# Kernel optimization log

Hardware: AMD Instinct MI355X
Metric: run time of the kernel (lower is better)

Reference implementation:

```python
import jax, jax.numpy as jnp
import numpy as np

B, A, L, D, H = 8, 16, 80, 128, 6  # scenes, agents/scene, lanes/scene, feat dim, heads
LN_EPS = 1e-5


def _build_edges():
    hi_l, wi_l = [], []
    n_agt = B * A
    for b in range(B):
        ids = np.concatenate([np.arange(b * A, (b + 1) * A),
                              n_agt + np.arange(b * L, (b + 1) * L)])
        n = len(ids)
        hi_l.append(np.repeat(ids, n))  # 'd -> (d n)'
        wi_l.append(np.tile(ids, n))    # 'd -> (n d)'
    return (jnp.asarray(np.concatenate(hi_l), dtype=jnp.int32),
            jnp.asarray(np.concatenate(wi_l), dtype=jnp.int32))


def setup_inputs() -> dict:
    key = jax.random.key(0)
    ks = jax.random.split(key, 10)
    w = 0.05  # small init so exp(att) is well-behaved
    hi, wi = _build_edges()
    return {
        "agents": jax.random.normal(ks[0], (B * A, D), jnp.float32),
        "lanes": jax.random.normal(ks[1], (B * L, D), jnp.float32),
        "Wq": w * jax.random.normal(ks[2], (D, H * D), jnp.float32),
        "Wk": w * jax.random.normal(ks[3], (D, H * D), jnp.float32),
        "Wv": w * jax.random.normal(ks[4], (D, H * D), jnp.float32),
        "Wout1": w * jax.random.normal(ks[5], (H * D, D), jnp.float32),
        "Wout2": w * jax.random.normal(ks[6], (D, D), jnp.float32),
        "W1": w * jax.random.normal(ks[7], (D, D), jnp.float32),
        "ln_g": jnp.ones((D,), jnp.float32),
        "ln_b": jnp.zeros((D,), jnp.float32),
        "W2": w * jax.random.normal(ks[8], (D, D), jnp.float32),
        "hi": hi,
        "wi": wi,
    }


def _layernorm(x, g, b):
    mu = x.mean(-1, keepdims=True)
    var = ((x - mu) ** 2).mean(-1, keepdims=True)
    return (x - mu) * jax.lax.rsqrt(var + LN_EPS) * g + b


def reference(agents, lanes, Wq, Wk, Wv, Wout1, Wout2, W1, ln_g, ln_b, W2, hi, wi):
    nodes = jnp.concatenate([agents, lanes], axis=0)  # [N, D]
    N = nodes.shape[0]
    n_agt = agents.shape[0]
    scale = D ** -0.5

    src = nodes[hi]  # [E, D] (query side)
    dst = nodes[wi]  # [E, D] (key/value side)
    q = (src @ Wq).reshape(-1, H, D)
    k = (dst @ Wk).reshape(-1, H, D)
    v = jax.nn.relu(dst @ Wv).reshape(-1, H, D)

    att = jnp.einsum('ehd,ehd->eh', q, k) * scale          # [E, H]
    att = jnp.exp(att - att.max())                          # global-max-shifted exp (as in source)
    denom = jax.ops.segment_sum(att, hi, num_segments=N)    # [N, H]
    att = att / denom[hi]
    out = jax.ops.segment_sum(att[..., None] * v, hi, num_segments=N)  # [N, H, D]
    out = out.reshape(N, H * D)

    out = jax.nn.relu(out @ Wout1) @ Wout2                  # to_out
    h = _layernorm(nodes @ W1 + out, ln_g, ln_b)
    h = jax.nn.relu(h)
    h = h @ W2
    h = jax.nn.relu(h + nodes)                              # residual to pre-attention nodes
    return h[:n_agt]
```

## Files before the change

kernel.cpp:

```cpp
#include <hip/hip_runtime.h>
#include <math.h>

#define LN_EPS 1e-5f


__global__ __launch_bounds__(256) void k_qv(
    const float* __restrict__ agents, const float* __restrict__ lanes,
    const float* __restrict__ Wv, const float* __restrict__ Wq,
    float* __restrict__ V, float* __restrict__ Qb)
{
    __shared__ float As[128][68];
    __shared__ float Bs[128][68];

    const int tid = threadIdx.x;
    const int bid = blockIdx.x;

    const float* W;
    float* Out;
    int r0, wc0;
    bool dorelu = false;
    if (bid < 144) {
        const int br = bid % 12, bc = bid / 12;
        r0 = br * 64; W = Wv; wc0 = bc * 64;
        Out = V; dorelu = true;
    } else {
        const int idx = bid - 144;
        r0 = (idx & 1) * 64; W = Wq; wc0 = (idx >> 1) * 64;
        Out = Qb;
    }

    {
        const int row = tid >> 2, kv = tid & 3;
        const int gr = r0 + row;
        const float* src = (gr < 128) ? (agents + (size_t)gr * 128)
                                      : (lanes + (size_t)(gr - 128) * 128);
        #pragma unroll
        for (int j = 0; j < 8; ++j) {
            const int k0 = kv * 4 + j * 16;
            const float4 a = *(const float4*)(src + k0);
            As[k0 + 0][row] = a.x; As[k0 + 1][row] = a.y;
            As[k0 + 2][row] = a.z; As[k0 + 3][row] = a.w;
        }
    }
    {
        const int kr = tid >> 4, c4 = tid & 15;
        #pragma unroll
        for (int i = 0; i < 8; ++i) {
            const int k = kr + 16 * i;
            *(float4*)&Bs[k][c4 * 4] =
                *(const float4*)(W + (size_t)k * 768 + wc0 + c4 * 4);
        }
    }
    __syncthreads();

    const int tx = tid & 15, ty = tid >> 4;
    float acc[4][4] = {};
    #pragma unroll 8
    for (int k = 0; k < 128; ++k) {
        const float4 a = *(const float4*)&As[k][ty * 4];
        const float4 b = *(const float4*)&Bs[k][tx * 4];
        const float av[4] = {a.x, a.y, a.z, a.w};
        #pragma unroll
        for (int i = 0; i < 4; ++i) {
            acc[i][0] += av[i] * b.x; acc[i][1] += av[i] * b.y;
            acc[i][2] += av[i] * b.z; acc[i][3] += av[i] * b.w;
        }
    }
    #pragma unroll
    for (int i = 0; i < 4; ++i) {
        float4 v = make_float4(acc[i][0], acc[i][1], acc[i][2], acc[i][3]);
        if (dorelu) {
            v.x = fmaxf(v.x, 0.f); v.y = fmaxf(v.y, 0.f);
            v.z = fmaxf(v.z, 0.f); v.w = fmaxf(v.w, 0.f);
        }
        *(float4*)(Out + (size_t)(r0 + ty * 4 + i) * 768 + wc0 + tx * 4) = v;
    }
}

__global__ __launch_bounds__(512) void k_attn(
    const float* __restrict__ agents, const float* __restrict__ lanes,
    const float* __restrict__ Wk, const float* __restrict__ V,
    const float* __restrict__ Qb, float* __restrict__ AO)
{
    __shared__ float Ns[96][132];
    __shared__ float Vh[96][64];
    __shared__ float Qs[16][132];
    __shared__ float Tt[16][132];
    __shared__ float Wks[128][132];
    float (*Sm)[100] = (float (*)[100])&Wks[0][0];

    const int tid = threadIdx.x;
    const int b = blockIdx.x;
    const int s = b / 12, r12 = b % 12;
    const int h = r12 >> 1, half = r12 & 1;

    #pragma unroll
    for (int ii = 0; ii < 6; ++ii) {
        const int idx = tid + ii * 512;
        const int n = idx >> 5, c4 = idx & 31;
        const float* src = (n < 16) ? (agents + (size_t)(s * 16 + n) * 128)
                                    : (lanes + (size_t)(s * 80 + n - 16) * 128);
        *(float4*)&Ns[n][c4 * 4] = *(const float4*)(src + c4 * 4);
    }
    #pragma unroll
    for (int ii = 0; ii < 8; ++ii) {
        const int idx = tid + ii * 512;
        const int row = idx >> 5, c4 = idx & 31;
        *(float4*)&Wks[row][c4 * 4] =
            *(const float4*)(Wk + (size_t)row * 768 + h * 128 + c4 * 4);
    }
    #pragma unroll
    for (int ii = 0; ii < 3; ++ii) {
        const int idx = tid + ii * 512;
        const int n = idx >> 4, c4 = idx & 15;
        const int g = (n < 16) ? (s * 16 + n) : (128 + s * 80 + (n - 16));
        *(float4*)&Vh[n][c4 * 4] =
            *(const float4*)(V + (size_t)g * 768 + h * 128 + half * 64 + c4 * 4);
    }
    {
        const int r = tid >> 5, c4 = tid & 31;
        *(float4*)&Qs[r][c4 * 4] =
            *(const float4*)(Qb + (size_t)(s * 16 + r) * 768 + h * 128 + c4 * 4);
    }
    __syncthreads();

    if (tid < 128) {
        const int kc = tid & 31, rq = tid >> 5;
        float acc[4][4] = {};
        #pragma unroll 4
        for (int c4 = 0; c4 < 32; ++c4) {
            float4 q[4], w[4];
            #pragma unroll
            for (int u = 0; u < 4; ++u)
                q[u] = *(const float4*)&Qs[rq + 4 * u][c4 * 4];
            #pragma unroll
            for (int u = 0; u < 4; ++u)
                w[u] = *(const float4*)&Wks[kc + 32 * u][c4 * 4];
            #pragma unroll
            for (int ur = 0; ur < 4; ++ur)
                #pragma unroll
                for (int uk = 0; uk < 4; ++uk)
                    acc[ur][uk] += q[ur].x * w[uk].x + q[ur].y * w[uk].y
                                 + q[ur].z * w[uk].z + q[ur].w * w[uk].w;
        }
        #pragma unroll
        for (int ur = 0; ur < 4; ++ur)
            #pragma unroll
            for (int uk = 0; uk < 4; ++uk)
                Tt[rq + 4 * ur][kc + 32 * uk] = acc[ur][uk];
    }
    __syncthreads();

    if (tid < 128) {
        const int jc = tid & 31, iq = tid >> 5;
        float s0[4] = {}, s1[4] = {}, s2[4] = {};
        #pragma unroll 4
        for (int kk = 0; kk < 32; ++kk) {
            float4 t[4];
            #pragma unroll
            for (int u = 0; u < 4; ++u)
                t[u] = *(const float4*)&Tt[iq + 4 * u][kk * 4];
            const float4 n0 = *(const float4*)&Ns[jc][kk * 4];
            const float4 n1 = *(const float4*)&Ns[jc + 32][kk * 4];
            const float4 n2 = *(const float4*)&Ns[jc + 64][kk * 4];
            #pragma unroll
            for (int u = 0; u < 4; ++u) {
                s0[u] += t[u].x*n0.x + t[u].y*n0.y + t[u].z*n0.z + t[u].w*n0.w;
                s1[u] += t[u].x*n1.x + t[u].y*n1.y + t[u].z*n1.z + t[u].w*n1.w;
                s2[u] += t[u].x*n2.x + t[u].y*n2.y + t[u].z*n2.z + t[u].w*n2.w;
            }
        }
        const float scale = 0.088388347648318447f;
        #pragma unroll
        for (int u = 0; u < 4; ++u) {
            const float a0 = s0[u] * scale, a1 = s1[u] * scale, a2 = s2[u] * scale;
            float m = fmaxf(fmaxf(a0, a1), a2);
            #pragma unroll
            for (int o = 16; o >= 1; o >>= 1) m = fmaxf(m, __shfl_xor(m, o, 32));
            const float e0 = __expf(a0 - m), e1 = __expf(a1 - m), e2 = __expf(a2 - m);
            float sum = e0 + e1 + e2;
            #pragma unroll
            for (int o = 16; o >= 1; o >>= 1) sum += __shfl_xor(sum, o, 32);
            const float inv = 1.0f / sum;
            Sm[iq + 4 * u][jc]      = e0 * inv;
            Sm[iq + 4 * u][jc + 32] = e1 * inv;
            Sm[iq + 4 * u][jc + 64] = e2 * inv;
        }
    }
    __syncthreads();

    if (tid < 64) {
        const int d4 = tid & 15, iq = tid >> 4;
        float4 acc[4] = {};
        #pragma unroll 2
        for (int j = 0; j < 96; ++j) {
            const float4 v = *(const float4*)&Vh[j][d4 * 4];
            #pragma unroll
            for (int u = 0; u < 4; ++u) {
                const float p = Sm[iq + 4 * u][j];
                acc[u].x += p * v.x; acc[u].y += p * v.y;
                acc[u].z += p * v.z; acc[u].w += p * v.w;
            }
        }
        #pragma unroll
        for (int u = 0; u < 4; ++u)
            *(float4*)(AO + (size_t)(s * 16 + iq + 4 * u) * 768 +
                       h * 128 + half * 64 + d4 * 4) = acc[u];
    }
}

__global__ __launch_bounds__(512) void k_tail(
    const float* __restrict__ AO, const float* __restrict__ agents,
    const float* __restrict__ Wout1, const float* __restrict__ Wout2,
    const float* __restrict__ W1, const float* __restrict__ ln_g,
    const float* __restrict__ ln_b, const float* __restrict__ W2,
    float* __restrict__ out)
{
    __shared__ float ao[768];
    __shared__ float nrs[128];
    __shared__ float ps[2048];
    __shared__ float y1s[128];
    __shared__ float hb[128];
    __shared__ float red[4];

    const int a = blockIdx.x, tid = threadIdx.x;
    if (tid < 192) {
        *(float4*)&ao[tid * 4] = *(const float4*)(AO + (size_t)a * 768 + tid * 4);
    } else if (tid < 224) {
        const int t = tid - 192;
        *(float4*)&nrs[t * 4] = *(const float4*)(agents + (size_t)a * 128 + t * 4);
    }
    __syncthreads();

    const int d4 = tid & 31, g = tid >> 5;
    {
        float4 acc = make_float4(0, 0, 0, 0);
        const int k0 = g * 48;
        #pragma unroll 8
        for (int k = 0; k < 48; ++k) {
            const float av = ao[k0 + k];
            const float4 w = *(const float4*)(Wout1 + (size_t)(k0 + k) * 128 + d4 * 4);
            acc.x += av * w.x; acc.y += av * w.y;
            acc.z += av * w.z; acc.w += av * w.w;
        }
        *(float4*)&ps[g * 128 + d4 * 4] = acc;
    }
    __syncthreads();
    if (tid < 128) {
        float ssum = 0.f;
        #pragma unroll
        for (int gg = 0; gg < 16; ++gg) ssum += ps[gg * 128 + tid];
        y1s[tid] = fmaxf(ssum, 0.f);
    }
    __syncthreads();
    {
        float4 acc = make_float4(0, 0, 0, 0);
        const int k0 = g * 8;
        #pragma unroll
        for (int k = 0; k < 8; ++k) {
            const float yv = y1s[k0 + k], nv = nrs[k0 + k];
            const float4 w2v = *(const float4*)(Wout2 + (size_t)(k0 + k) * 128 + d4 * 4);
            const float4 w1v = *(const float4*)(W1 + (size_t)(k0 + k) * 128 + d4 * 4);
            acc.x += yv * w2v.x + nv * w1v.x; acc.y += yv * w2v.y + nv * w1v.y;
            acc.z += yv * w2v.z + nv * w1v.z; acc.w += yv * w2v.w + nv * w1v.w;
        }
        *(float4*)&ps[g * 128 + d4 * 4] = acc;
    }
    __syncthreads();
    float tval = 0.f;
    if (tid < 128) {
        #pragma unroll
        for (int gg = 0; gg < 16; ++gg) tval += ps[gg * 128 + tid];
    }
    float s1 = tval, s2 = tval * tval;
    #pragma unroll
    for (int o = 32; o >= 1; o >>= 1) { s1 += __shfl_xor(s1, o); s2 += __shfl_xor(s2, o); }
    if (tid < 128 && (tid & 63) == 0) {
        red[(tid >> 6) * 2] = s1; red[(tid >> 6) * 2 + 1] = s2;
    }
    __syncthreads();
    if (tid < 128) {
        const float S1 = red[0] + red[2], S2 = red[1] + red[3];
        const float mu  = S1 * (1.0f / 128.0f);
        const float var = S2 * (1.0f / 128.0f) - mu * mu;
        hb[tid] = fmaxf((tval - mu) * rsqrtf(var + LN_EPS) * ln_g[tid] + ln_b[tid], 0.f);
    }
    __syncthreads();
    {
        float4 acc = make_float4(0, 0, 0, 0);
        const int k0 = g * 8;
        #pragma unroll
        for (int k = 0; k < 8; ++k) {
            const float hv = hb[k0 + k];
            const float4 w = *(const float4*)(W2 + (size_t)(k0 + k) * 128 + d4 * 4);
            acc.x += hv * w.x; acc.y += hv * w.y;
            acc.z += hv * w.z; acc.w += hv * w.w;
        }
        *(float4*)&ps[g * 128 + d4 * 4] = acc;
    }
    __syncthreads();
    if (tid < 128) {
        float o_ = nrs[tid];
        #pragma unroll
        for (int gg = 0; gg < 16; ++gg) o_ += ps[gg * 128 + tid];
        out[(size_t)a * 128 + tid] = fmaxf(o_, 0.f);
    }
}

extern "C" void kernel_launch(void* const* d_in, const int* in_sizes, int n_in,
                              void* d_out, int out_size, void* d_ws, size_t ws_size,
                              hipStream_t stream)
{
    const float* agents = (const float*)d_in[0];
    const float* lanes  = (const float*)d_in[1];
    const float* Wq     = (const float*)d_in[2];
    const float* Wk     = (const float*)d_in[3];
    const float* Wv     = (const float*)d_in[4];
    const float* Wout1  = (const float*)d_in[5];
    const float* Wout2  = (const float*)d_in[6];
    const float* W1     = (const float*)d_in[7];
    const float* ln_g   = (const float*)d_in[8];
    const float* ln_b   = (const float*)d_in[9];
    const float* W2     = (const float*)d_in[10];

    float* ws = (float*)d_ws;
    float* V    = ws;
    float* Qb   = V + 768 * 768;
    float* AO   = Qb + 128 * 768;
    float* outp = (float*)d_out;

    k_qv  <<<168, 256, 0, stream>>>(agents, lanes, Wv, Wq, V, Qb);
    k_attn<<<96, 512, 0, stream>>>(agents, lanes, Wk, V, Qb, AO);
    k_tail<<<128, 512, 0, stream>>>(AO, agents, Wout1, Wout2, W1, ln_g, ln_b, W2, outp);
}
```

Baseline: 112.4 us.

## Fuse three kernels into one persistent kernel with atomic-counter grid barriers

Merges the QV projection, attention and tail kernels into a single launch of 168 blocks. Stages are separated by global atomic counters and spin-waits, with a shared-memory union reused across stages. The Wk and node loads are issued before the wait so they overlap the projection stage. The tail now handles two agents per block, and the probability matrix is stored transposed so the PV loop can use vector reads. This removes two kernel-launch gaps, but adds a memset launch and relies on all 168 blocks being co-resident for the spin barrier to be safe.

```diff
diff --git a/kernel.cpp b/kernel.cpp
--- a/kernel.cpp
+++ b/kernel.cpp
@@ -4,94 +4,109 @@
 #define LN_EPS 1e-5f
 
 
-__global__ __launch_bounds__(256) void k_qv(
+union SmemU {
+    struct {
+        float As[128][68];
+        float Bs[128][68];
+    } a;
+    struct {
+        float Ns[96][132];
+        float Wks[128][132];
+        float Vh[96][64];
+        float Qs[16][132];
+        float Tt[16][132];
+    } b;
+    struct {
+        float ao0[768], ao1[768];
+        float nr0[128], nr1[128];
+        float ps0[2048], ps1[2048];
+        float y10[128], y11[128];
+        float hb0[128], hb1[128];
+        float red[8];
+    } c;
+};
+
+__global__ __launch_bounds__(512) void k_all(
     const float* __restrict__ agents, const float* __restrict__ lanes,
-    const float* __restrict__ Wv, const float* __restrict__ Wq,
-    float* __restrict__ V, float* __restrict__ Qb)
+    const float* __restrict__ Wq, const float* __restrict__ Wk,
+    const float* __restrict__ Wv, const float* __restrict__ Wout1,
+    const float* __restrict__ Wout2, const float* __restrict__ W1,
+    const float* __restrict__ ln_g, const float* __restrict__ ln_b,
+    const float* __restrict__ W2, float* __restrict__ V,
+    float* __restrict__ Qb, float* __restrict__ AO,
+    int* __restrict__ cnts, float* __restrict__ out)
 {
-    __shared__ float As[128][68];
-    __shared__ float Bs[128][68];
-
+    __shared__ SmemU sm;
     const int tid = threadIdx.x;
     const int bid = blockIdx.x;
 
-    const float* W;
-    float* Out;
-    int r0, wc0;
-    bool dorelu = false;
-    if (bid < 144) {
-        const int br = bid % 12, bc = bid / 12;
-        r0 = br * 64; W = Wv; wc0 = bc * 64;
-        Out = V; dorelu = true;
+    if (tid < 256) {
+        const float* W;
+        float* Out;
+        int r0, wc0;
+        bool dorelu = false;
+        if (bid < 144) {
+            const int br = bid % 12, bc = bid / 12;
+            r0 = br * 64; W = Wv; wc0 = bc * 64; Out = V; dorelu = true;
+        } else {
+            const int idx = bid - 144;
+            r0 = (idx & 1) * 64; W = Wq; wc0 = (idx >> 1) * 64; Out = Qb;
+        }
+        {
+            const int row = tid >> 2, kv = tid & 3;
+            const int gr = r0 + row;
+            const float* src = (gr < 128) ? (agents + (size_t)gr * 128)
+                                          : (lanes + (size_t)(gr - 128) * 128);
+            #pragma unroll
+            for (int j = 0; j < 8; ++j) {
+                const int k0 = kv * 4 + j * 16;
+                const float4 a = *(const float4*)(src + k0);
+                sm.a.As[k0 + 0][row] = a.x; sm.a.As[k0 + 1][row] = a.y;
+                sm.a.As[k0 + 2][row] = a.z; sm.a.As[k0 + 3][row] = a.w;
+            }
+        }
+        {
+            const int kr = tid >> 4, c4 = tid & 15;
+            #pragma unroll
+            for (int i = 0; i < 8; ++i) {
+                const int k = kr + 16 * i;
+                *(float4*)&sm.a.Bs[k][c4 * 4] =
+                    *(const float4*)(W + (size_t)k * 768 + wc0 + c4 * 4);
+            }
+        }
+        __syncthreads();
+        const int tx = tid & 15, ty = tid >> 4;
+        float acc[4][4] = {};
+        #pragma unroll 8
+        for (int k = 0; k < 128; ++k) {
+            const float4 a = *(const float4*)&sm.a.As[k][ty * 4];
+            const float4 b = *(const float4*)&sm.a.Bs[k][tx * 4];
+            const float av[4] = {a.x, a.y, a.z, a.w};
+            #pragma unroll
+            for (int i = 0; i < 4; ++i) {
+                acc[i][0] += av[i] * b.x; acc[i][1] += av[i] * b.y;
+                acc[i][2] += av[i] * b.z; acc[i][3] += av[i] * b.w;
+            }
+        }
+        #pragma unroll
+        for (int i = 0; i < 4; ++i) {
+            float4 v = make_float4(acc[i][0], acc[i][1], acc[i][2], acc[i][3]);
+            if (dorelu) {
+                v.x = fmaxf(v.x, 0.f); v.y = fmaxf(v.y, 0.f);
+                v.z = fmaxf(v.z, 0.f); v.w = fmaxf(v.w, 0.f);
+            }
+            *(float4*)(Out + (size_t)(r0 + ty * 4 + i) * 768 + wc0 + tx * 4) = v;
+        }
     } else {
-        const int idx = bid - 144;
-        r0 = (idx & 1) * 64; W = Wq; wc0 = (idx >> 1) * 64;
-        Out = Qb;
-    }
-
-    {
-        const int row = tid >> 2, kv = tid & 3;
-        const int gr = r0 + row;
-        const float* src = (gr < 128) ? (agents + (size_t)gr * 128)
-                                      : (lanes + (size_t)(gr - 128) * 128);
-        #pragma unroll
-        for (int j = 0; j < 8; ++j) {
-            const int k0 = kv * 4 + j * 16;
-            const float4 a = *(const float4*)(src + k0);
-            As[k0 + 0][row] = a.x; As[k0 + 1][row] = a.y;
-            As[k0 + 2][row] = a.z; As[k0 + 3][row] = a.w;
-        }
-    }
-    {
-        const int kr = tid >> 4, c4 = tid & 15;
-        #pragma unroll
-        for (int i = 0; i < 8; ++i) {
-            const int k = kr + 16 * i;
-            *(float4*)&Bs[k][c4 * 4] =
-                *(const float4*)(W + (size_t)k * 768 + wc0 + c4 * 4);
-        }
-    }
-    __syncthreads();
-
-    const int tx = tid & 15, ty = tid >> 4;
-    float acc[4][4] = {};
-    #pragma unroll 8
-    for (int k = 0; k < 128; ++k) {
-        const float4 a = *(const float4*)&As[k][ty * 4];
-        const float4 b = *(const float4*)&Bs[k][tx * 4];
-        const float av[4] = {a.x, a.y, a.z, a.w};
-        #pragma unroll
-        for (int i = 0; i < 4; ++i) {
-            acc[i][0] += av[i] * b.x; acc[i][1] += av[i] * b.y;
-            acc[i][2] += av[i] * b.z; acc[i][3] += av[i] * b.w;
-        }
-    }
-    #pragma unroll
-    for (int i = 0; i < 4; ++i) {
-        float4 v = make_float4(acc[i][0], acc[i][1], acc[i][2], acc[i][3]);
-        if (dorelu) {
-            v.x = fmaxf(v.x, 0.f); v.y = fmaxf(v.y, 0.f);
-            v.z = fmaxf(v.z, 0.f); v.w = fmaxf(v.w, 0.f);
-        }
-        *(float4*)(Out + (size_t)(r0 + ty * 4 + i) * 768 + wc0 + tx * 4) = v;
-    }
-}
-
-__global__ __launch_bounds__(512) void k_attn(
-    const float* __restrict__ agents, const float* __restrict__ lanes,
-    const float* __restrict__ Wk, const float* __restrict__ V,
-    const float* __restrict__ Qb, float* __restrict__ AO)
-{
-    __shared__ float Ns[96][132];
-    __shared__ float Vh[96][64];
-    __shared__ float Qs[16][132];
-    __shared__ float Tt[16][132];
-    __shared__ float Wks[128][132];
-    float (*Sm)[100] = (float (*)[100])&Wks[0][0];
-
-    const int tid = threadIdx.x;
-    const int b = blockIdx.x;
-    const int s = b / 12, r12 = b % 12;
+        __syncthreads();
+    }
+
+    __threadfence();
+    __syncthreads();
+    if (tid == 0) atomicAdd(&cnts[0], 1);
+    if (bid >= 96) return;
+
+    const int s = bid / 12, r12 = bid % 12;
     const int h = r12 >> 1, half = r12 & 1;
 
     #pragma unroll
@@ -100,26 +115,36 @@
         const int n = idx >> 5, c4 = idx & 31;
         const float* src = (n < 16) ? (agents + (size_t)(s * 16 + n) * 128)
                                     : (lanes + (size_t)(s * 80 + n - 16) * 128);
-        *(float4*)&Ns[n][c4 * 4] = *(const float4*)(src + c4 * 4);
+        *(float4*)&sm.b.Ns[n][c4 * 4] = *(const float4*)(src + c4 * 4);
     }
     #pragma unroll
     for (int ii = 0; ii < 8; ++ii) {
         const int idx = tid + ii * 512;
         const int row = idx >> 5, c4 = idx & 31;
-        *(float4*)&Wks[row][c4 * 4] =
+        *(float4*)&sm.b.Wks[row][c4 * 4] =
             *(const float4*)(Wk + (size_t)row * 768 + h * 128 + c4 * 4);
     }
+
+    if (tid == 0) {
+        int guard = 0;
+        while (atomicAdd(&cnts[0], 0) < 168 && guard < 10000000) {
+            __builtin_amdgcn_s_sleep(2); ++guard;
+        }
+    }
+    __syncthreads();
+    __threadfence();
+
     #pragma unroll
     for (int ii = 0; ii < 3; ++ii) {
         const int idx = tid + ii * 512;
         const int n = idx >> 4, c4 = idx & 15;
         const int g = (n < 16) ? (s * 16 + n) : (128 + s * 80 + (n - 16));
-        *(float4*)&Vh[n][c4 * 4] =
+        *(float4*)&sm.b.Vh[n][c4 * 4] =
             *(const float4*)(V + (size_t)g * 768 + h * 128 + half * 64 + c4 * 4);
     }
     {
         const int r = tid >> 5, c4 = tid & 31;
-        *(float4*)&Qs[r][c4 * 4] =
+        *(float4*)&sm.b.Qs[r][c4 * 4] =
             *(const float4*)(Qb + (size_t)(s * 16 + r) * 768 + h * 128 + c4 * 4);
     }
     __syncthreads();
@@ -132,10 +157,10 @@
             float4 q[4], w[4];
             #pragma unroll
             for (int u = 0; u < 4; ++u)
-                q[u] = *(const float4*)&Qs[rq + 4 * u][c4 * 4];
+                q[u] = *(const float4*)&sm.b.Qs[rq + 4 * u][c4 * 4];
             #pragma unroll
             for (int u = 0; u < 4; ++u)
-                w[u] = *(const float4*)&Wks[kc + 32 * u][c4 * 4];
+                w[u] = *(const float4*)&sm.b.Wks[kc + 32 * u][c4 * 4];
             #pragma unroll
             for (int ur = 0; ur < 4; ++ur)
                 #pragma unroll
@@ -147,10 +172,11 @@
         for (int ur = 0; ur < 4; ++ur)
             #pragma unroll
             for (int uk = 0; uk < 4; ++uk)
-                Tt[rq + 4 * ur][kc + 32 * uk] = acc[ur][uk];
-    }
-    __syncthreads();
-
+                sm.b.Tt[rq + 4 * ur][kc + 32 * uk] = acc[ur][uk];
+    }
+    __syncthreads();
+
+    float (*Sm)[20] = (float (*)[20])&sm.b.Wks[0][0];
     if (tid < 128) {
         const int jc = tid & 31, iq = tid >> 5;
         float s0[4] = {}, s1[4] = {}, s2[4] = {};
@@ -159,10 +185,10 @@
             float4 t[4];
             #pragma unroll
             for (int u = 0; u < 4; ++u)
-                t[u] = *(const float4*)&Tt[iq + 4 * u][kk * 4];
-            const float4 n0 = *(const float4*)&Ns[jc][kk * 4];
-            const float4 n1 = *(const float4*)&Ns[jc + 32][kk * 4];
-            const float4 n2 = *(const float4*)&Ns[jc + 64][kk * 4];
+                t[u] = *(const float4*)&sm.b.Tt[iq + 4 * u][kk * 4];
+            const float4 n0 = *(const float4*)&sm.b.Ns[jc][kk * 4];
+            const float4 n1 = *(const float4*)&sm.b.Ns[jc + 32][kk * 4];
+            const float4 n2 = *(const float4*)&sm.b.Ns[jc + 64][kk * 4];
             #pragma unroll
             for (int u = 0; u < 4; ++u) {
                 s0[u] += t[u].x*n0.x + t[u].y*n0.y + t[u].z*n0.z + t[u].w*n0.w;
@@ -182,9 +208,10 @@
             #pragma unroll
             for (int o = 16; o >= 1; o >>= 1) sum += __shfl_xor(sum, o, 32);
             const float inv = 1.0f / sum;
-            Sm[iq + 4 * u][jc]      = e0 * inv;
-            Sm[iq + 4 * u][jc + 32] = e1 * inv;
-            Sm[iq + 4 * u][jc + 64] = e2 * inv;
+            const int i = iq + 4 * u;
+            Sm[jc][i]      = e0 * inv;
+            Sm[jc + 32][i] = e1 * inv;
+            Sm[jc + 64][i] = e2 * inv;
         }
     }
     __syncthreads();
@@ -194,116 +221,145 @@
         float4 acc[4] = {};
         #pragma unroll 2
         for (int j = 0; j < 96; ++j) {
-            const float4 v = *(const float4*)&Vh[j][d4 * 4];
+            const float4 p = *(const float4*)&Sm[j][iq * 4];
+            const float4 v = *(const float4*)&sm.b.Vh[j][d4 * 4];
+            const float pv[4] = {p.x, p.y, p.z, p.w};
             #pragma unroll
             for (int u = 0; u < 4; ++u) {
-                const float p = Sm[iq + 4 * u][j];
-                acc[u].x += p * v.x; acc[u].y += p * v.y;
-                acc[u].z += p * v.z; acc[u].w += p * v.w;
+                acc[u].x += pv[u] * v.x; acc[u].y += pv[u] * v.y;
+                acc[u].z += pv[u] * v.z; acc[u].w += pv[u] * v.w;
             }
         }
         #pragma unroll
         for (int u = 0; u < 4; ++u)
-            *(float4*)(AO + (size_t)(s * 16 + iq + 4 * u) * 768 +
+            *(float4*)(AO + (size_t)(s * 16 + iq * 4 + u) * 768 +
                        h * 128 + half * 64 + d4 * 4) = acc[u];
     }
-}
-
-__global__ __launch_bounds__(512) void k_tail(
-    const float* __restrict__ AO, const float* __restrict__ agents,
-    const float* __restrict__ Wout1, const float* __restrict__ Wout2,
-    const float* __restrict__ W1, const float* __restrict__ ln_g,
-    const float* __restrict__ ln_b, const float* __restrict__ W2,
-    float* __restrict__ out)
-{
-    __shared__ float ao[768];
-    __shared__ float nrs[128];
-    __shared__ float ps[2048];
-    __shared__ float y1s[128];
-    __shared__ float hb[128];
-    __shared__ float red[4];
-
-    const int a = blockIdx.x, tid = threadIdx.x;
+
+    __threadfence();
+    __syncthreads();
+    if (tid == 0) atomicAdd(&cnts[1 + s], 1);
+    if (r12 >= 8) return;
+
+    if (tid == 0) {
+        int guard = 0;
+        while (atomicAdd(&cnts[1 + s], 0) < 12 && guard < 10000000) {
+            __builtin_amdgcn_s_sleep(2); ++guard;
+        }
+    }
+    __syncthreads();
+    __threadfence();
+
+    const int a0 = s * 16 + r12 * 2, a1 = a0 + 1;
     if (tid < 192) {
-        *(float4*)&ao[tid * 4] = *(const float4*)(AO + (size_t)a * 768 + tid * 4);
-    } else if (tid < 224) {
+        *(float4*)&sm.c.ao0[tid * 4] = *(const float4*)(AO + (size_t)a0 * 768 + tid * 4);
+    } else if (tid < 384) {
         const int t = tid - 192;
-        *(float4*)&nrs[t * 4] = *(const float4*)(agents + (size_t)a * 128 + t * 4);
+        *(float4*)&sm.c.ao1[t * 4] = *(const float4*)(AO + (size_t)a1 * 768 + t * 4);
+    } else if (tid < 416) {
+        const int t = tid - 384;
+        *(float4*)&sm.c.nr0[t * 4] = *(const float4*)(agents + (size_t)a0 * 128 + t * 4);
+    } else if (tid < 448) {
+        const int t = tid - 416;
+        *(float4*)&sm.c.nr1[t * 4] = *(const float4*)(agents + (size_t)a1 * 128 + t * 4);
     }
     __syncthreads();
 
     const int d4 = tid & 31, g = tid >> 5;
     {
-        float4 acc = make_float4(0, 0, 0, 0);
+        float4 acc0 = make_float4(0, 0, 0, 0), acc1 = make_float4(0, 0, 0, 0);
         const int k0 = g * 48;
         #pragma unroll 8
         for (int k = 0; k < 48; ++k) {
-            const float av = ao[k0 + k];
             const float4 w = *(const float4*)(Wout1 + (size_t)(k0 + k) * 128 + d4 * 4);
-            acc.x += av * w.x; acc.y += av * w.y;
-            acc.z += av * w.z; acc.w += av * w.w;
-        }
-        *(float4*)&ps[g * 128 + d4 * 4] = acc;
-    }
-    __syncthreads();
-    if (tid < 128) {
-        float ssum = 0.f;
-        #pragma unroll
-        for (int gg = 0; gg < 16; ++gg) ssum += ps[gg * 128 + tid];
-        y1s[tid] = fmaxf(ssum, 0.f);
+            const float v0 = sm.c.ao0[k0 + k], v1 = sm.c.ao1[k0 + k];
+            acc0.x += v0 * w.x; acc0.y += v0 * w.y; acc0.z += v0 * w.z; acc0.w += v0 * w.w;
+            acc1.x += v1 * w.x; acc1.y += v1 * w.y; acc1.z += v1 * w.z; acc1.w += v1 * w.w;
+        }
+        *(float4*)&sm.c.ps0[g * 128 + d4 * 4] = acc0;
+        *(float4*)&sm.c.ps1[g * 128 + d4 * 4] = acc1;
+    }
+    __syncthreads();
+    if (tid < 128) {
+        float u0 = 0.f, u1 = 0.f;
+        #pragma unroll
+        for (int gg = 0; gg < 16; ++gg) {
+            u0 += sm.c.ps0[gg * 128 + tid]; u1 += sm.c.ps1[gg * 128 + tid];
+        }
+        sm.c.y10[tid] = fmaxf(u0, 0.f); sm.c.y11[tid] = fmaxf(u1, 0.f);
     }
     __syncthreads();
     {
-        float4 acc = make_float4(0, 0, 0, 0);
+        float4 acc0 = make_float4(0, 0, 0, 0), acc1 = make_float4(0, 0, 0, 0);
         const int k0 = g * 8;
         #pragma unroll
         for (int k = 0; k < 8; ++k) {
-            const float yv = y1s[k0 + k], nv = nrs[k0 + k];
             const float4 w2v = *(const float4*)(Wout2 + (size_t)(k0 + k) * 128 + d4 * 4);
             const float4 w1v = *(const float4*)(W1 + (size_t)(k0 + k) * 128 + d4 * 4);
-            acc.x += yv * w2v.x + nv * w1v.x; acc.y += yv * w2v.y + nv * w1v.y;
-            acc.z += yv * w2v.z + nv * w1v.z; acc.w += yv * w2v.w + nv * w1v.w;
-        }
-        *(float4*)&ps[g * 128 + d4 * 4] = acc;
-    }
-    __syncthreads();
-    float tval = 0.f;
-    if (tid < 128) {
-        #pragma unroll
-        for (int gg = 0; gg < 16; ++gg) tval += ps[gg * 128 + tid];
-    }
-    float s1 = tval, s2 = tval * tval;
+            const float y0 = sm.c.y10[k0 + k], n0 = sm.c.nr0[k0 + k];
+            const float y1 = sm.c.y11[k0 + k], n1 = sm.c.nr1[k0 + k];
+            acc0.x += y0 * w2v.x + n0 * w1v.x; acc0.y += y0 * w2v.y + n0 * w1v.y;
+            acc0.z += y0 * w2v.z + n0 * w1v.z; acc0.w += y0 * w2v.w + n0 * w1v.w;
+            acc1.x += y1 * w2v.x + n1 * w1v.x; acc1.y += y1 * w2v.y + n1 * w1v.y;
+            acc1.z += y1 * w2v.z + n1 * w1v.z; acc1.w += y1 * w2v.w + n1 * w1v.w;
+        }
+        *(float4*)&sm.c.ps0[g * 128 + d4 * 4] = acc0;
+        *(float4*)&sm.c.ps1[g * 128 + d4 * 4] = acc1;
+    }
+    __syncthreads();
+    float t0 = 0.f, t1 = 0.f;
+    if (tid < 128) {
+        #pragma unroll
+        for (int gg = 0; gg < 16; ++gg) {
+            t0 += sm.c.ps0[gg * 128 + tid]; t1 += sm.c.ps1[gg * 128 + tid];
+        }
+    }
+    float s10 = t0, s20 = t0 * t0, s11 = t1, s21 = t1 * t1;
     #pragma unroll
-    for (int o = 32; o >= 1; o >>= 1) { s1 += __shfl_xor(s1, o); s2 += __shfl_xor(s2, o); }
+    for (int o = 32; o >= 1; o >>= 1) {
+        s10 += __shfl_xor(s10, o); s20 += __shfl_xor(s20, o);
+        s11 += __shfl_xor(s11, o); s21 += __shfl_xor(s21, o);
+    }
     if (tid < 128 && (tid & 63) == 0) {
-        red[(tid >> 6) * 2] = s1; red[(tid >> 6) * 2 + 1] = s2;
-    }
-    __syncthreads();
-    if (tid < 128) {
-        const float S1 = red[0] + red[2], S2 = red[1] + red[3];
-        const float mu  = S1 * (1.0f / 128.0f);
-        const float var = S2 * (1.0f / 128.0f) - mu * mu;
-        hb[tid] = fmaxf((tval - mu) * rsqrtf(var + LN_EPS) * ln_g[tid] + ln_b[tid], 0.f);
+        const int wid = tid >> 6;
+        sm.c.red[wid * 4 + 0] = s10; sm.c.red[wid * 4 + 1] = s20;
+        sm.c.red[wid * 4 + 2] = s11; sm.c.red[wid * 4 + 3] = s21;
+    }
+    __syncthreads();
+    if (tid < 128) {
+        const float S10 = sm.c.red[0] + sm.c.red[4], S20 = sm.c.red[1] + sm.c.red[5];
+        const float S11 = sm.c.red[2] + sm.c.red[6], S21 = sm.c.red[3] + sm.c.red[7];
+        const float mu0 = S10 * (1.0f / 128.0f);
+        const float var0 = S20 * (1.0f / 128.0f) - mu0 * mu0;
+        const float mu1 = S11 * (1.0f / 128.0f);
+        const float var1 = S21 * (1.0f / 128.0f) - mu1 * mu1;
+        const float g_ = ln_g[tid], b_ = ln_b[tid];
+        sm.c.hb0[tid] = fmaxf((t0 - mu0) * rsqrtf(var0 + LN_EPS) * g_ + b_, 0.0f);
+        sm.c.hb1[tid] = fmaxf((t1 - mu1) * rsqrtf(var1 + LN_EPS) * g_ + b_, 0.0f);
     }
     __syncthreads();
     {
-        float4 acc = make_float4(0, 0, 0, 0);
+        float4 acc0 = make_float4(0, 0, 0, 0), acc1 = make_float4(0, 0, 0, 0);
         const int k0 = g * 8;
         #pragma unroll
         for (int k = 0; k < 8; ++k) {
-            const float hv = hb[k0 + k];
             const float4 w = *(const float4*)(W2 + (size_t)(k0 + k) * 128 + d4 * 4);
-            acc.x += hv * w.x; acc.y += hv * w.y;
-            acc.z += hv * w.z; acc.w += hv * w.w;
-        }
-        *(float4*)&ps[g * 128 + d4 * 4] = acc;
-    }
-    __syncthreads();
-    if (tid < 128) {
-        float o_ = nrs[tid];
-        #pragma unroll
-        for (int gg = 0; gg < 16; ++gg) o_ += ps[gg * 128 + tid];
-        out[(size_t)a * 128 + tid] = fmaxf(o_, 0.f);
+            const float v0 = sm.c.hb0[k0 + k], v1 = sm.c.hb1[k0 + k];
+            acc0.x += v0 * w.x; acc0.y += v0 * w.y; acc0.z += v0 * w.z; acc0.w += v0 * w.w;
+            acc1.x += v1 * w.x; acc1.y += v1 * w.y; acc1.z += v1 * w.z; acc1.w += v1 * w.w;
+        }
+        *(float4*)&sm.c.ps0[g * 128 + d4 * 4] = acc0;
+        *(float4*)&sm.c.ps1[g * 128 + d4 * 4] = acc1;
+    }
+    __syncthreads();
+    if (tid < 128) {
+        float o0 = sm.c.nr0[tid], o1 = sm.c.nr1[tid];
+        #pragma unroll
+        for (int gg = 0; gg < 16; ++gg) {
+            o0 += sm.c.ps0[gg * 128 + tid]; o1 += sm.c.ps1[gg * 128 + tid];
+        }
+        out[(size_t)a0 * 128 + tid] = fmaxf(o0, 0.f);
+        out[(size_t)a1 * 128 + tid] = fmaxf(o1, 0.f);
     }
 }
 
@@ -327,9 +383,10 @@
     float* V    = ws;
     float* Qb   = V + 768 * 768;
     float* AO   = Qb + 128 * 768;
+    int*   cnts = (int*)(AO + 128 * 768);
     float* outp = (float*)d_out;
 
-    k_qv  <<<168, 256, 0, stream>>>(agents, lanes, Wv, Wq, V, Qb);
-    k_attn<<<96, 512, 0, stream>>>(agents, lanes, Wk, V, Qb, AO);
-    k_tail<<<128, 512, 0, stream>>>(AO, agents, Wout1, Wout2, W1, ln_g, ln_b, W2, outp);
+    hipMemsetAsync(cnts, 0, 64, stream);
+    k_all<<<168, 512, 0, stream>>>(agents, lanes, Wq, Wk, Wv, Wout1, Wout2,
+                                   W1, ln_g, ln_b, W2, V, Qb, AO, cnts, outp);
 }
```

Measured after the change: 169.5 us. +50.8%, slower.

## Fuse Q/V projections into attention kernel and process two agents per tail block

Applied to the files above, without the earlier changes.

Removes the separate k_qv GEMM kernel and instead computes the per-scene V slice (with ReLU) and the Q rows inside each attention block from shared-memory node features and weights. This drops a kernel launch and the global round-trip of V and Q through the workspace. It also recomputes the Q projection in both half-blocks of each head. The softmax-probability matrix is stored transposed so the PV loop reads probabilities as float4, and the tail kernel handles two agents per block so each weight load is reused across both.

```diff
diff --git a/kernel.cpp b/kernel.cpp
--- a/kernel.cpp
+++ b/kernel.cpp
@@ -4,90 +4,19 @@
 #define LN_EPS 1e-5f
 
 
-__global__ __launch_bounds__(256) void k_qv(
-    const float* __restrict__ agents, const float* __restrict__ lanes,
-    const float* __restrict__ Wv, const float* __restrict__ Wq,
-    float* __restrict__ V, float* __restrict__ Qb)
-{
-    __shared__ float As[128][68];
-    __shared__ float Bs[128][68];
-
-    const int tid = threadIdx.x;
-    const int bid = blockIdx.x;
-
-    const float* W;
-    float* Out;
-    int r0, wc0;
-    bool dorelu = false;
-    if (bid < 144) {
-        const int br = bid % 12, bc = bid / 12;
-        r0 = br * 64; W = Wv; wc0 = bc * 64;
-        Out = V; dorelu = true;
-    } else {
-        const int idx = bid - 144;
-        r0 = (idx & 1) * 64; W = Wq; wc0 = (idx >> 1) * 64;
-        Out = Qb;
-    }
-
-    {
-        const int row = tid >> 2, kv = tid & 3;
-        const int gr = r0 + row;
-        const float* src = (gr < 128) ? (agents + (size_t)gr * 128)
-                                      : (lanes + (size_t)(gr - 128) * 128);
-        #pragma unroll
-        for (int j = 0; j < 8; ++j) {
-            const int k0 = kv * 4 + j * 16;
-            const float4 a = *(const float4*)(src + k0);
-            As[k0 + 0][row] = a.x; As[k0 + 1][row] = a.y;
-            As[k0 + 2][row] = a.z; As[k0 + 3][row] = a.w;
-        }
-    }
-    {
-        const int kr = tid >> 4, c4 = tid & 15;
-        #pragma unroll
-        for (int i = 0; i < 8; ++i) {
-            const int k = kr + 16 * i;
-            *(float4*)&Bs[k][c4 * 4] =
-                *(const float4*)(W + (size_t)k * 768 + wc0 + c4 * 4);
-        }
-    }
-    __syncthreads();
-
-    const int tx = tid & 15, ty = tid >> 4;
-    float acc[4][4] = {};
-    #pragma unroll 8
-    for (int k = 0; k < 128; ++k) {
-        const float4 a = *(const float4*)&As[k][ty * 4];
-        const float4 b = *(const float4*)&Bs[k][tx * 4];
-        const float av[4] = {a.x, a.y, a.z, a.w};
-        #pragma unroll
-        for (int i = 0; i < 4; ++i) {
-            acc[i][0] += av[i] * b.x; acc[i][1] += av[i] * b.y;
-            acc[i][2] += av[i] * b.z; acc[i][3] += av[i] * b.w;
-        }
-    }
-    #pragma unroll
-    for (int i = 0; i < 4; ++i) {
-        float4 v = make_float4(acc[i][0], acc[i][1], acc[i][2], acc[i][3]);
-        if (dorelu) {
-            v.x = fmaxf(v.x, 0.f); v.y = fmaxf(v.y, 0.f);
-            v.z = fmaxf(v.z, 0.f); v.w = fmaxf(v.w, 0.f);
-        }
-        *(float4*)(Out + (size_t)(r0 + ty * 4 + i) * 768 + wc0 + tx * 4) = v;
-    }
-}
-
 __global__ __launch_bounds__(512) void k_attn(
     const float* __restrict__ agents, const float* __restrict__ lanes,
-    const float* __restrict__ Wk, const float* __restrict__ V,
-    const float* __restrict__ Qb, float* __restrict__ AO)
+    const float* __restrict__ Wq, const float* __restrict__ Wk,
+    const float* __restrict__ Wv, float* __restrict__ AO)
 {
-    __shared__ float Ns[96][132];
-    __shared__ float Vh[96][64];
-    __shared__ float Qs[16][132];
-    __shared__ float Tt[16][132];
-    __shared__ float Wks[128][132];
-    float (*Sm)[100] = (float (*)[100])&Wks[0][0];
+    __shared__ float smem[40384];
+    float (*Ns)[132]  = (float (*)[132])(smem);
+    float (*Wks)[132] = (float (*)[132])(smem + 12672);
+    float (*Wvh)[68]  = (float (*)[68]) (smem + 29568);
+    float (*Tt)[132]  = (float (*)[132])(smem + 38272);
+    float (*Vh)[68]   = (float (*)[68]) (smem + 29568);
+    float (*Qs)[132]  = (float (*)[132])(smem + 36096);
+    float (*Sm)[20]   = (float (*)[20]) (smem + 12672);
 
     const int tid = threadIdx.x;
     const int b = blockIdx.x;
@@ -110,29 +39,83 @@
             *(const float4*)(Wk + (size_t)row * 768 + h * 128 + c4 * 4);
     }
     #pragma unroll
-    for (int ii = 0; ii < 3; ++ii) {
+    for (int ii = 0; ii < 4; ++ii) {
         const int idx = tid + ii * 512;
-        const int n = idx >> 4, c4 = idx & 15;
-        const int g = (n < 16) ? (s * 16 + n) : (128 + s * 80 + (n - 16));
-        *(float4*)&Vh[n][c4 * 4] =
-            *(const float4*)(V + (size_t)g * 768 + h * 128 + half * 64 + c4 * 4);
-    }
-    {
-        const int r = tid >> 5, c4 = tid & 31;
-        *(float4*)&Qs[r][c4 * 4] =
-            *(const float4*)(Qb + (size_t)(s * 16 + r) * 768 + h * 128 + c4 * 4);
-    }
-    __syncthreads();
-
-    if (tid < 128) {
-        const int kc = tid & 31, rq = tid >> 5;
+        const int row = idx >> 4, c4 = idx & 15;
+        *(float4*)&Wvh[row][c4 * 4] =
+            *(const float4*)(Wv + (size_t)row * 768 + h * 128 + half * 64 + c4 * 4);
+    }
+    __syncthreads();
+
+    float4 vacc[6];
+    float4 qacc0 = make_float4(0, 0, 0, 0), qacc1 = make_float4(0, 0, 0, 0);
+    int vr = 0, vc4 = 0, qc = 0, qrg = 0;
+    if (tid < 256) {
+        vc4 = tid & 15; vr = tid >> 4;
+        #pragma unroll
+        for (int u = 0; u < 6; ++u) vacc[u] = make_float4(0, 0, 0, 0);
+        #pragma unroll 2
+        for (int k4 = 0; k4 < 32; ++k4) {
+            float4 w[4];
+            #pragma unroll
+            for (int j = 0; j < 4; ++j)
+                w[j] = *(const float4*)&Wvh[k4 * 4 + j][vc4 * 4];
+            #pragma unroll
+            for (int u = 0; u < 6; ++u) {
+                const float4 nv = *(const float4*)&Ns[vr + 16 * u][k4 * 4];
+                vacc[u].x += nv.x*w[0].x + nv.y*w[1].x + nv.z*w[2].x + nv.w*w[3].x;
+                vacc[u].y += nv.x*w[0].y + nv.y*w[1].y + nv.z*w[2].y + nv.w*w[3].y;
+                vacc[u].z += nv.x*w[0].z + nv.y*w[1].z + nv.z*w[2].z + nv.w*w[3].z;
+                vacc[u].w += nv.x*w[0].w + nv.y*w[1].w + nv.z*w[2].w + nv.w*w[3].w;
+            }
+        }
+    } else {
+        const int t = tid - 256;
+        qc = t & 31; qrg = t >> 5;
+        const float* wp = Wq + (size_t)h * 128 + qc * 4;
+        #pragma unroll 2
+        for (int k4 = 0; k4 < 32; ++k4) {
+            float4 w[4];
+            #pragma unroll
+            for (int j = 0; j < 4; ++j)
+                w[j] = *(const float4*)(wp + (size_t)(k4 * 4 + j) * 768);
+            const float4 n0 = *(const float4*)&Ns[2 * qrg][k4 * 4];
+            const float4 n1 = *(const float4*)&Ns[2 * qrg + 1][k4 * 4];
+            qacc0.x += n0.x*w[0].x + n0.y*w[1].x + n0.z*w[2].x + n0.w*w[3].x;
+            qacc0.y += n0.x*w[0].y + n0.y*w[1].y + n0.z*w[2].y + n0.w*w[3].y;
+            qacc0.z += n0.x*w[0].z + n0.y*w[1].z + n0.z*w[2].z + n0.w*w[3].z;
+            qacc0.w += n0.x*w[0].w + n0.y*w[1].w + n0.z*w[2].w + n0.w*w[3].w;
+            qacc1.x += n1.x*w[0].x + n1.y*w[1].x + n1.z*w[2].x + n1.w*w[3].x;
+            qacc1.y += n1.x*w[0].y + n1.y*w[1].y + n1.z*w[2].y + n1.w*w[3].y;
+            qacc1.z += n1.x*w[0].z + n1.y*w[1].z + n1.z*w[2].z + n1.w*w[3].z;
+            qacc1.w += n1.x*w[0].w + n1.y*w[1].w + n1.z*w[2].w + n1.w*w[3].w;
+        }
+    }
+    __syncthreads();
+
+    if (tid < 256) {
+        #pragma unroll
+        for (int u = 0; u < 6; ++u) {
+            float4 v = vacc[u];
+            v.x = fmaxf(v.x, 0.f); v.y = fmaxf(v.y, 0.f);
+            v.z = fmaxf(v.z, 0.f); v.w = fmaxf(v.w, 0.f);
+            *(float4*)&Vh[vr + 16 * u][vc4 * 4] = v;
+        }
+    } else {
+        *(float4*)&Qs[2 * qrg][qc * 4]     = qacc0;
+        *(float4*)&Qs[2 * qrg + 1][qc * 4] = qacc1;
+    }
+    __syncthreads();
+
+    const int r = tid >> 5, kc = tid & 31;
+    if (tid < 128) {
         float acc[4][4] = {};
         #pragma unroll 4
         for (int c4 = 0; c4 < 32; ++c4) {
             float4 q[4], w[4];
             #pragma unroll
             for (int u = 0; u < 4; ++u)
-                q[u] = *(const float4*)&Qs[rq + 4 * u][c4 * 4];
+                q[u] = *(const float4*)&Qs[r + 4 * u][c4 * 4];
             #pragma unroll
             for (int u = 0; u < 4; ++u)
                 w[u] = *(const float4*)&Wks[kc + 32 * u][c4 * 4];
@@ -147,12 +130,12 @@
         for (int ur = 0; ur < 4; ++ur)
             #pragma unroll
             for (int uk = 0; uk < 4; ++uk)
-                Tt[rq + 4 * ur][kc + 32 * uk] = acc[ur][uk];
-    }
-    __syncthreads();
-
-    if (tid < 128) {
-        const int jc = tid & 31, iq = tid >> 5;
+                Tt[r + 4 * ur][kc + 32 * uk] = acc[ur][uk];
+    }
+    __syncthreads();
+
+    if (tid < 128) {
+        const int jc = kc, iq = r;
         float s0[4] = {}, s1[4] = {}, s2[4] = {};
         #pragma unroll 4
         for (int kk = 0; kk < 32; ++kk) {
@@ -182,9 +165,10 @@
             #pragma unroll
             for (int o = 16; o >= 1; o >>= 1) sum += __shfl_xor(sum, o, 32);
             const float inv = 1.0f / sum;
-            Sm[iq + 4 * u][jc]      = e0 * inv;
-            Sm[iq + 4 * u][jc + 32] = e1 * inv;
-            Sm[iq + 4 * u][jc + 64] = e2 * inv;
+            const int i = iq + 4 * u;
+            Sm[jc][i]      = e0 * inv;
+            Sm[jc + 32][i] = e1 * inv;
+            Sm[jc + 64][i] = e2 * inv;
         }
     }
     __syncthreads();
@@ -194,17 +178,18 @@
         float4 acc[4] = {};
         #pragma unroll 2
         for (int j = 0; j < 96; ++j) {
+            const float4 p = *(const float4*)&Sm[j][iq * 4];
             const float4 v = *(const float4*)&Vh[j][d4 * 4];
+            const float pv[4] = {p.x, p.y, p.z, p.w};
             #pragma unroll
             for (int u = 0; u < 4; ++u) {
-                const float p = Sm[iq + 4 * u][j];
-                acc[u].x += p * v.x; acc[u].y += p * v.y;
-                acc[u].z += p * v.z; acc[u].w += p * v.w;
+                acc[u].x += pv[u] * v.x; acc[u].y += pv[u] * v.y;
+                acc[u].z += pv[u] * v.z; acc[u].w += pv[u] * v.w;
             }
         }
         #pragma unroll
         for (int u = 0; u < 4; ++u)
-            *(float4*)(AO + (size_t)(s * 16 + iq + 4 * u) * 768 +
+            *(float4*)(AO + (size_t)(s * 16 + iq * 4 + u) * 768 +
                        h * 128 + half * 64 + d4 * 4) = acc[u];
     }
 }
@@ -216,94 +201,125 @@
     const float* __restrict__ ln_b, const float* __restrict__ W2,
     float* __restrict__ out)
 {
-    __shared__ float ao[768];
-    __shared__ float nrs[128];
-    __shared__ float ps[2048];
-    __shared__ float y1s[128];
-    __shared__ float hb[128];
-    __shared__ float red[4];
-
-    const int a = blockIdx.x, tid = threadIdx.x;
+    __shared__ float ao0[768], ao1[768];
+    __shared__ float nr0[128], nr1[128];
+    __shared__ float ps0[2048], ps1[2048];
+    __shared__ float y10[128], y11[128];
+    __shared__ float hb0[128], hb1[128];
+    __shared__ float red[8];
+
+    const int tid = threadIdx.x;
+    const int a0 = blockIdx.x * 2, a1 = a0 + 1;
+
     if (tid < 192) {
-        *(float4*)&ao[tid * 4] = *(const float4*)(AO + (size_t)a * 768 + tid * 4);
-    } else if (tid < 224) {
+        *(float4*)&ao0[tid * 4] = *(const float4*)(AO + (size_t)a0 * 768 + tid * 4);
+    } else if (tid < 384) {
         const int t = tid - 192;
-        *(float4*)&nrs[t * 4] = *(const float4*)(agents + (size_t)a * 128 + t * 4);
+        *(float4*)&ao1[t * 4] = *(const float4*)(AO + (size_t)a1 * 768 + t * 4);
+    } else if (tid < 416) {
+        const int t = tid - 384;
+        *(float4*)&nr0[t * 4] = *(const float4*)(agents + (size_t)a0 * 128 + t * 4);
+    } else if (tid < 448) {
+        const int t = tid - 416;
+        *(float4*)&nr1[t * 4] = *(const float4*)(agents + (size_t)a1 * 128 + t * 4);
     }
     __syncthreads();
 
     const int d4 = tid & 31, g = tid >> 5;
     {
-        float4 acc = make_float4(0, 0, 0, 0);
+        float4 acc0 = make_float4(0, 0, 0, 0), acc1 = make_float4(0, 0, 0, 0);
         const int k0 = g * 48;
         #pragma unroll 8
         for (int k = 0; k < 48; ++k) {
-            const float av = ao[k0 + k];
             const float4 w = *(const float4*)(Wout1 + (size_t)(k0 + k) * 128 + d4 * 4);
-            acc.x += av * w.x; acc.y += av * w.y;
-            acc.z += av * w.z; acc.w += av * w.w;
-        }
-        *(float4*)&ps[g * 128 + d4 * 4] = acc;
-    }
-    __syncthreads();
-    if (tid < 128) {
-        float ssum = 0.f;
-        #pragma unroll
-        for (int gg = 0; gg < 16; ++gg) ssum += ps[gg * 128 + tid];
-        y1s[tid] = fmaxf(ssum, 0.f);
+            const float v0 = ao0[k0 + k], v1 = ao1[k0 + k];
+            acc0.x += v0 * w.x; acc0.y += v0 * w.y; acc0.z += v0 * w.z; acc0.w += v0 * w.w;
+            acc1.x += v1 * w.x; acc1.y += v1 * w.y; acc1.z += v1 * w.z; acc1.w += v1 * w.w;
+        }
+        *(float4*)&ps0[g * 128 + d4 * 4] = acc0;
+        *(float4*)&ps1[g * 128 + d4 * 4] = acc1;
+    }
+    __syncthreads();
+    if (tid < 128) {
+        float u0 = 0.f, u1 = 0.f;
+        #pragma unroll
+        for (int gg = 0; gg < 16; ++gg) {
+            u0 += ps0[gg * 128 + tid]; u1 += ps1[gg * 128 + tid];
+        }
+        y10[tid] = fmaxf(u0, 0.f); y11[tid] = fmaxf(u1, 0.f);
     }
     __syncthreads();
     {
-        float4 acc = make_float4(0, 0, 0, 0);
+        float4 acc0 = make_float4(0, 0, 0, 0), acc1 = make_float4(0, 0, 0, 0);
         const int k0 = g * 8;
         #pragma unroll
         for (int k = 0; k < 8; ++k) {
-            const float yv = y1s[k0 + k], nv = nrs[k0 + k];
             const float4 w2v = *(const float4*)(Wout2 + (size_t)(k0 + k) * 128 + d4 * 4);
             const float4 w1v = *(const float4*)(W1 + (size_t)(k0 + k) * 128 + d4 * 4);
-            acc.x += yv * w2v.x + nv * w1v.x; acc.y += yv * w2v.y + nv * w1v.y;
-            acc.z += yv * w2v.z + nv * w1v.z; acc.w += yv * w2v.w + nv * w1v.w;
-        }
-        *(float4*)&ps[g * 128 + d4 * 4] = acc;
-    }
-    __syncthreads();
-    float tval = 0.f;
-    if (tid < 128) {
-        #pragma unroll
-        for (int gg = 0; gg < 16; ++gg) tval += ps[gg * 128 + tid];
-    }
-    float s1 = tval, s2 = tval * tval;
+            const float v0 = y10[k0 + k], n0 = nr0[k0 + k];
+            const float v1 = y11[k0 + k], n1 = nr1[k0 + k];
+            acc0.x += v0 * w2v.x + n0 * w1v.x; acc0.y += v0 * w2v.y + n0 * w1v.y;
+            acc0.z += v0 * w2v.z + n0 * w1v.z; acc0.w += v0 * w2v.w + n0 * w1v.w;
+            acc1.x += v1 * w2v.x + n1 * w1v.x; acc1.y += v1 * w2v.y + n1 * w1v.y;
+            acc1.z += v1 * w2v.z + n1 * w1v.z; acc1.w += v1 * w2v.w + n1 * w1v.w;
+        }
+        *(float4*)&ps0[g * 128 + d4 * 4] = acc0;
+        *(float4*)&ps1[g * 128 + d4 * 4] = acc1;
+    }
+    __syncthreads();
+    float t0 = 0.f, t1 = 0.f;
+    if (tid < 128) {
+        #pragma unroll
+        for (int gg = 0; gg < 16; ++gg) {
+            t0 += ps0[gg * 128 + tid]; t1 += ps1[gg * 128 + tid];
+        }
+    }
+    float s10 = t0, s20 = t0 * t0, s11 = t1, s21 = t1 * t1;
     #pragma unroll
-    for (int o = 32; o >= 1; o >>= 1) { s1 += __shfl_xor(s1, o); s2 += __shfl_xor(s2, o); }
+    for (int o = 32; o >= 1; o >>= 1) {
+        s10 += __shfl_xor(s10, o); s20 += __shfl_xor(s20, o);
+        s11 += __shfl_xor(s11, o); s21 += __shfl_xor(s21, o);
+    }
     if (tid < 128 && (tid & 63) == 0) {
-        red[(tid >> 6) * 2] = s1; red[(tid >> 6) * 2 + 1] = s2;
-    }
-    __syncthreads();
-    if (tid < 128) {
-        const float S1 = red[0] + red[2], S2 = red[1] + red[3];
-        const float mu  = S1 * (1.0f / 128.0f);
-        const float var = S2 * (1.0f / 128.0f) - mu * mu;
-        hb[tid] = fmaxf((tval - mu) * rsqrtf(var + LN_EPS) * ln_g[tid] + ln_b[tid], 0.f);
+        const int wid = tid >> 6;
+        red[wid * 4 + 0] = s10; red[wid * 4 + 1] = s20;
+        red[wid * 4 + 2] = s11; red[wid * 4 + 3] = s21;
+    }
+    __syncthreads();
+    if (tid < 128) {
+        const float S10 = red[0] + red[4], S20 = red[1] + red[5];
+        const float S11 = red[2] + red[6], S21 = red[3] + red[7];
+        const float mu0 = S10 * (1.0f / 128.0f);
+        const float var0 = S20 * (1.0f / 128.0f) - mu0 * mu0;
+        const float mu1 = S11 * (1.0f / 128.0f);
+        const float var1 = S21 * (1.0f / 128.0f) - mu1 * mu1;
+        const float g_ = ln_g[tid], b_ = ln_b[tid];
+        hb0[tid] = fmaxf((t0 - mu0) * rsqrtf(var0 + LN_EPS) * g_ + b_, 0.0f);
+        hb1[tid] = fmaxf((t1 - mu1) * rsqrtf(var1 + LN_EPS) * g_ + b_, 0.0f);
     }
     __syncthreads();
     {
-        float4 acc = make_float4(0, 0, 0, 0);
+        float4 acc0 = make_float4(0, 0, 0, 0), acc1 = make_float4(0, 0, 0, 0);
         const int k0 = g * 8;
         #pragma unroll
         for (int k = 0; k < 8; ++k) {
-            const float hv = hb[k0 + k];
             const float4 w = *(const float4*)(W2 + (size_t)(k0 + k) * 128 + d4 * 4);
-            acc.x += hv * w.x; acc.y += hv * w.y;
-            acc.z += hv * w.z; acc.w += hv * w.w;
-        }
-        *(float4*)&ps[g * 128 + d4 * 4] = acc;
-    }
-    __syncthreads();
-    if (tid < 128) {
-        float o_ = nrs[tid];
-        #pragma unroll
-        for (int gg = 0; gg < 16; ++gg) o_ += ps[gg * 128 + tid];
-        out[(size_t)a * 128 + tid] = fmaxf(o_, 0.f);
+            const float v0 = hb0[k0 + k], v1 = hb1[k0 + k];
+            acc0.x += v0 * w.x; acc0.y += v0 * w.y; acc0.z += v0 * w.z; acc0.w += v0 * w.w;
+            acc1.x += v1 * w.x; acc1.y += v1 * w.y; acc1.z += v1 * w.z; acc1.w += v1 * w.w;
+        }
+        *(float4*)&ps0[g * 128 + d4 * 4] = acc0;
+        *(float4*)&ps1[g * 128 + d4 * 4] = acc1;
+    }
+    __syncthreads();
+    if (tid < 128) {
+        float o0 = nr0[tid], o1 = nr1[tid];
+        #pragma unroll
+        for (int gg = 0; gg < 16; ++gg) {
+            o0 += ps0[gg * 128 + tid]; o1 += ps1[gg * 128 + tid];
+        }
+        out[(size_t)a0 * 128 + tid] = fmaxf(o0, 0.f);
+        out[(size_t)a1 * 128 + tid] = fmaxf(o1, 0.f);
     }
 }
 
@@ -323,13 +339,10 @@
     const float* ln_b   = (const float*)d_in[9];
     const float* W2     = (const float*)d_in[10];
 
-    float* ws = (float*)d_ws;
-    float* V    = ws;
-    float* Qb   = V + 768 * 768;
-    float* AO   = Qb + 128 * 768;
+    float* AO   = (float*)d_ws;
     float* outp = (float*)d_out;
 
-    k_qv  <<<168, 256, 0, stream>>>(agents, lanes, Wv, Wq, V, Qb);
-    k_attn<<<96, 512, 0, stream>>>(agents, lanes, Wk, V, Qb, AO);
-    k_tail<<<128, 512, 0, stream>>>(AO, agents, Wout1, Wout2, W1, ln_g, ln_b, W2, outp);
+    k_attn<<<96, 512, 0, stream>>>(agents, lanes, Wq, Wk, Wv, AO);
+    k_tail<<<64, 512, 0, stream>>>(AO, agents, Wout1, Wout2, W1,
+                                   ln_g, ln_b, W2, outp);
 }
```

Measured after the change: 113.1 us. No clear change (+0.6%).
